# Kernel optimization log

Hardware: AMD Instinct MI355X
Metric: run time of the kernel (lower is better)

Reference implementation:

```python
import jax, jax.numpy as jnp
import numpy as np
from jax import lax

B, T, K = 32, 2048, 1024


def setup_inputs() -> dict:
    key = jax.random.key(0)
    x = jax.random.normal(key, (B, T, K), dtype=jnp.float32)
    return {"x": x}


def reference(x) -> jnp.ndarray:
    # x: [B, T, K]. Max-plus DP:
    #   out[:, 0]   = x[:, 0]
    #   out[:, i+1] = x[:, i+1] + max(out[:, i], shift_right(out[:, i], -inf))
    neg_inf = jnp.asarray(-jnp.inf, dtype=x.dtype)
    x_t = jnp.swapaxes(x, 0, 1)  # [T, B, K] time-major for scan

    def step(carry, xi):
        # carry: [B, K] = out row i; xi: [B, K] = x row i+1
        shifted = jnp.concatenate(
            [jnp.full_like(carry[:, :1], neg_inf), carry[:, :-1]], axis=1
        )
        new = xi + jnp.maximum(carry, shifted)
        return new, new

    init = x_t[0]
    _, rows = lax.scan(step, init, x_t[1:])  # rows: [T-1, B, K]
    out = jnp.concatenate([init[None], rows], axis=0)  # [T, B, K]
    return jnp.swapaxes(out, 0, 1)  # [B, T, K]
```

## Files before the change

### kernel.cpp

```cpp
#include <hip/hip_runtime.h>
#include <math.h>


#define BB 32
#define TT 2048
#define KK 1024
#define GG 8
#define WW (KK / GG)
#define RR 32
#define HH 16
#define NT (TT / RR)

typedef __attribute__((address_space(1))) void GV;
typedef __attribute__((address_space(3))) void LV;

#define BAR() do {                                              \
    __asm__ volatile("s_waitcnt lgkmcnt(0)" ::: "memory");      \
    __builtin_amdgcn_s_barrier();                               \
    __builtin_amdgcn_sched_barrier(0);                          \
} while (0)

__global__ __launch_bounds__(256, 1)
void harddtw_ws(const float* __restrict__ x, float* __restrict__ out,
                int* __restrict__ flags, float* __restrict__ bws)
{
    const int bid  = blockIdx.x;
    const int g    = bid >> 5;
    const int b    = bid & 31;
    const int w    = threadIdx.x >> 6;
    const int lane = threadIdx.x & 63;
    const bool lz  = (lane == 0);

    const int k0 = g * WW;
    const int kc = k0 + (lane << 1);
    const size_t base = (size_t)b * TT * KK;

    int* myflag = flags + bid;
    int* upflag = flags + bid - 32;
    float*       mybw = bws + ((size_t)(b * GG + g)) * TT;
    const float* upbw = bws + ((size_t)(b * GG + g - 1)) * TT;

    __shared__ float xbuf[2][RR * WW];
    __shared__ float obuf[2][HH * WW];

    const float* xstage = x + base + k0 + (size_t)(lane >> 5) * KK
                          + ((lane & 31) << 2);

    const bool pub = (g < GG - 1);

    float pv0 = 0.0f, pv1 = 0.0f;
    float sh_prev = 0.0f;
    float bcur = -INFINITY, bnxt = -INFINITY;
    int   bndv = 0;
    int   fpre = 0;

    if (w == 1) {
        const float* gp = xstage;
#pragma unroll
        for (int i = 0; i < RR / 2; ++i) {
            __builtin_amdgcn_global_load_lds((GV*)(void*)gp,
                                             (LV*)(void*)&xbuf[0][i * 256],
                                             16, 0, 0);
            gp += 2 * KK;
        }
        __asm__ volatile("s_waitcnt vmcnt(0)" ::: "memory");
    }
    if (w == 0 && g > 0) {
        while (__hip_atomic_load(upflag, __ATOMIC_RELAXED,
                                 __HIP_MEMORY_SCOPE_AGENT) < 1)
            __builtin_amdgcn_s_sleep(1);
        __asm__ volatile("" ::: "memory");
        if (lz) bcur = 0.0f;
        else if (lane < RR)
            bcur = __hip_atomic_load(upbw + lane - 1, __ATOMIC_RELAXED,
                                     __HIP_MEMORY_SCOPE_AGENT);
    }
    BAR();

#pragma unroll 1
    for (int r = 0; r < NT; ++r) {
        const int cur = r & 1;

        if (w == 0) {
            float2 td[HH];
#pragma unroll
            for (int j = 0; j < HH; ++j)
                td[j] = *(const float2*)&xbuf[cur][j * WW + (lane << 1)];
            __builtin_amdgcn_sched_barrier(0);
            float2 ov[HH];
#pragma unroll
            for (int j = 0; j < HH; ++j) {
                float2 xv = td[j];
                float n1 = xv.y + fmaxf(pv1, pv0);
                float sh_new = __shfl_up(n1, 1);
                float bv = __int_as_float(
                    __builtin_amdgcn_readlane(__float_as_int(bcur), j));
                float left = lz ? bv : sh_prev;
                float n0 = xv.x + fmaxf(pv0, left);
                ov[j].x = n0; ov[j].y = n1;
                {
                    int b63 = __builtin_amdgcn_readlane(__float_as_int(n1), 63);
                    if (lane == j) bndv = b63;
                }
                pv0 = n0; pv1 = n1; sh_prev = sh_new;
            }
#pragma unroll
            for (int j = 0; j < HH; ++j)
                *(float2*)&obuf[0][j * WW + (lane << 1)] = ov[j];
        } else if (w >= 2 && r > 0) {
            const int sw = w - 2;
            float* ob = out + base
                      + (size_t)((r - 1) * RR + HH + sw * 8) * KK + kc;
#pragma unroll
            for (int i = 0; i < 8; ++i) {
                float2 v = *(const float2*)&obuf[1][(sw * 8 + i) * WW
                                                    + (lane << 1)];
                *(float2*)ob = v;
                ob += KK;
            }
        }
        BAR();

        if (w == 0) {
            float2 td[HH];
#pragma unroll
            for (int j = 0; j < HH; ++j)
                td[j] = *(const float2*)&xbuf[cur][(HH + j) * WW + (lane << 1)];
            __builtin_amdgcn_sched_barrier(0);
            float2 ov[HH];
#pragma unroll
            for (int j = 0; j < HH; ++j) {
                float2 xv = td[j];
                float n1 = xv.y + fmaxf(pv1, pv0);
                float sh_new = __shfl_up(n1, 1);
                float bv = __int_as_float(
                    __builtin_amdgcn_readlane(__float_as_int(bcur), HH + j));
                float left = lz ? bv : sh_prev;
                float n0 = xv.x + fmaxf(pv0, left);
                ov[j].x = n0; ov[j].y = n1;
                {
                    int b63 = __builtin_amdgcn_readlane(__float_as_int(n1), 63);
                    if (lane == HH + j) bndv = b63;
                }
                pv0 = n0; pv1 = n1; sh_prev = sh_new;
            }
#pragma unroll
            for (int j = 0; j < HH; ++j)
                *(float2*)&obuf[1][j * WW + (lane << 1)] = ov[j];

            if (pub) {
                if (lane < RR)
                    __hip_atomic_store(mybw + (size_t)r * RR + lane,
                                       __int_as_float(bndv),
                                       __ATOMIC_RELAXED,
                                       __HIP_MEMORY_SCOPE_AGENT);
                __asm__ volatile("s_waitcnt vmcnt(0)" ::: "memory");
                if (lz)
                    __hip_atomic_store(myflag, r + 1, __ATOMIC_RELAXED,
                                       __HIP_MEMORY_SCOPE_AGENT);
            }
            if (g > 0 && r < NT - 1) {
                if (fpre < r + 2) {
                    while (__hip_atomic_load(upflag, __ATOMIC_RELAXED,
                                             __HIP_MEMORY_SCOPE_AGENT) < r + 2)
                        __builtin_amdgcn_s_sleep(1);
                }
                __asm__ volatile("" ::: "memory");
                if (lane < RR)
                    bnxt = __hip_atomic_load(
                               upbw + (size_t)(r + 1) * RR + lane - 1,
                               __ATOMIC_RELAXED, __HIP_MEMORY_SCOPE_AGENT);
                fpre = __hip_atomic_load(upflag, __ATOMIC_RELAXED,
                                         __HIP_MEMORY_SCOPE_AGENT);
            }
            bcur = bnxt;
        } else if (w == 1) {
            if (r < NT - 1) {
                const float* gp = xstage + (size_t)(r + 1) * RR * KK;
                float* lp = &xbuf[cur ^ 1][0];
#pragma unroll
                for (int i = 0; i < RR / 2; ++i) {
                    __builtin_amdgcn_global_load_lds((GV*)(void*)gp,
                                                     (LV*)(void*)(lp + i * 256),
                                                     16, 0, 0);
                    gp += 2 * KK;
                }
                __asm__ volatile("s_waitcnt vmcnt(0)" ::: "memory");
            }
        } else if (w >= 2) {
            const int sw = w - 2;
            float* ob = out + base + (size_t)(r * RR + sw * 8) * KK + kc;
#pragma unroll
            for (int i = 0; i < 8; ++i) {
                float2 v = *(const float2*)&obuf[0][(sw * 8 + i) * WW
                                                    + (lane << 1)];
                *(float2*)ob = v;
                ob += KK;
            }
        }
        BAR();
    }

    if (w >= 2) {
        const int sw = w - 2;
        float* ob = out + base
                  + (size_t)((NT - 1) * RR + HH + sw * 8) * KK + kc;
#pragma unroll
        for (int i = 0; i < 8; ++i) {
            float2 v = *(const float2*)&obuf[1][(sw * 8 + i) * WW
                                                + (lane << 1)];
            *(float2*)ob = v;
            ob += KK;
        }
    }
}

extern "C" void kernel_launch(void* const* d_in, const int* in_sizes, int n_in,
                              void* d_out, int out_size, void* d_ws, size_t ws_size,
                              hipStream_t stream) {
    (void)in_sizes; (void)n_in; (void)out_size; (void)ws_size;
    const float* x = (const float*)d_in[0];
    float* out = (float*)d_out;
    int* flags = (int*)d_ws;
    float* bws = (float*)((char*)d_ws + 4096);

    (void)hipMemsetAsync(flags, 0, BB * GG * sizeof(int), stream);

    harddtw_ws<<<dim3(BB * GG), dim3(256), 0, stream>>>(x, out, flags, bws);
}
```

Before: 557.0 us.

## Triple-buffer x tiles and defer boundary flag publish by one round

The LDS staging buffer for x grows from two to three tiles. The loader wave now prefetches two tiles ahead and waits only on the older batch (vmcnt(16)) instead of draining all loads before each barrier. The compute wave no longer drains all its stores before raising the boundary flag. It instead publishes the previous round's flag after a partial vmcnt wait, and does a final flag store after the loop. This takes global-memory latency off the serial per-round critical path. The cost is a downstream group sees boundary data one round later, which adds pipeline skew across the eight column groups.

```diff
diff --git a/kernel.cpp b/kernel.cpp
--- a/kernel.cpp
+++ b/kernel.cpp
@@ -21,8 +21,8 @@
 } while (0)
 
 __global__ __launch_bounds__(256, 1)
-void harddtw_ws(const float* __restrict__ x, float* __restrict__ out,
-                int* __restrict__ flags, float* __restrict__ bws)
+void harddtw_ws2(const float* __restrict__ x, float* __restrict__ out,
+                 int* __restrict__ flags, float* __restrict__ bws)
 {
     const int bid  = blockIdx.x;
     const int g    = bid >> 5;
@@ -40,7 +40,7 @@
     float*       mybw = bws + ((size_t)(b * GG + g)) * TT;
     const float* upbw = bws + ((size_t)(b * GG + g - 1)) * TT;
 
-    __shared__ float xbuf[2][RR * WW];
+    __shared__ float xbuf[3][RR * WW];
     __shared__ float obuf[2][HH * WW];
 
     const float* xstage = x + base + k0 + (size_t)(lane >> 5) * KK
@@ -55,13 +55,15 @@
     int   fpre = 0;
 
     if (w == 1) {
-        const float* gp = xstage;
-#pragma unroll
-        for (int i = 0; i < RR / 2; ++i) {
-            __builtin_amdgcn_global_load_lds((GV*)(void*)gp,
-                                             (LV*)(void*)&xbuf[0][i * 256],
-                                             16, 0, 0);
-            gp += 2 * KK;
+#pragma unroll
+        for (int t = 0; t < 2; ++t) {
+            const float* gp = xstage + (size_t)t * RR * KK;
+#pragma unroll
+            for (int i = 0; i < RR / 2; ++i) {
+                __builtin_amdgcn_global_load_lds(
+                    (GV*)(void*)gp, (LV*)(void*)&xbuf[t][i * 256], 16, 0, 0);
+                gp += 2 * KK;
+            }
         }
         __asm__ volatile("s_waitcnt vmcnt(0)" ::: "memory");
     }
@@ -79,7 +81,7 @@
 
 #pragma unroll 1
     for (int r = 0; r < NT; ++r) {
-        const int cur = r & 1;
+        const int cur = r % 3;
 
         if (w == 0) {
             float2 td[HH];
@@ -154,10 +156,15 @@
                                        __int_as_float(bndv),
                                        __ATOMIC_RELAXED,
                                        __HIP_MEMORY_SCOPE_AGENT);
-                __asm__ volatile("s_waitcnt vmcnt(0)" ::: "memory");
-                if (lz)
-                    __hip_atomic_store(myflag, r + 1, __ATOMIC_RELAXED,
-                                       __HIP_MEMORY_SCOPE_AGENT);
+                if (r > 0) {
+                    if (g > 0)
+                        __asm__ volatile("s_waitcnt vmcnt(3)" ::: "memory");
+                    else
+                        __asm__ volatile("s_waitcnt vmcnt(1)" ::: "memory");
+                    if (lz)
+                        __hip_atomic_store(myflag, r, __ATOMIC_RELAXED,
+                                           __HIP_MEMORY_SCOPE_AGENT);
+                }
             }
             if (g > 0 && r < NT - 1) {
                 if (fpre < r + 2) {
@@ -175,16 +182,17 @@
             }
             bcur = bnxt;
         } else if (w == 1) {
-            if (r < NT - 1) {
-                const float* gp = xstage + (size_t)(r + 1) * RR * KK;
-                float* lp = &xbuf[cur ^ 1][0];
+            if (r < NT - 2) {
+                const float* gp = xstage + (size_t)(r + 2) * RR * KK;
+                float* lp = &xbuf[(r + 2) % 3][0];
 #pragma unroll
                 for (int i = 0; i < RR / 2; ++i) {
-                    __builtin_amdgcn_global_load_lds((GV*)(void*)gp,
-                                                     (LV*)(void*)(lp + i * 256),
-                                                     16, 0, 0);
+                    __builtin_amdgcn_global_load_lds(
+                        (GV*)(void*)gp, (LV*)(void*)(lp + i * 256), 16, 0, 0);
                     gp += 2 * KK;
                 }
+                __asm__ volatile("s_waitcnt vmcnt(16)" ::: "memory");
+            } else {
                 __asm__ volatile("s_waitcnt vmcnt(0)" ::: "memory");
             }
         } else if (w >= 2) {
@@ -212,6 +220,12 @@
             *(float2*)ob = v;
             ob += KK;
         }
+    }
+    if (w == 0 && pub) {
+        __asm__ volatile("s_waitcnt vmcnt(0)" ::: "memory");
+        if (lz)
+            __hip_atomic_store(myflag, NT, __ATOMIC_RELAXED,
+                               __HIP_MEMORY_SCOPE_AGENT);
     }
 }
 
@@ -226,5 +240,5 @@
 
     (void)hipMemsetAsync(flags, 0, BB * GG * sizeof(int), stream);
 
-    harddtw_ws<<<dim3(BB * GG), dim3(256), 0, stream>>>(x, out, flags, bws);
+    harddtw_ws2<<<dim3(BB * GG), dim3(256), 0, stream>>>(x, out, flags, bws);
 }
```

Result: no change. 557.4 us (+0.1%).
